# Kernel tuning notes

Hardware: AMD Instinct MI355X
Metric: run time of the kernel (lower is better)

Reference implementation:

```python
import jax, jax.numpy as jnp
import numpy as np

B_, L_, D_ = 8, 2048, 1024      # batch, seq_len, d_model
E, DS, K = 2, 16, 4             # expand, d_state, d_conv
DI = E * D_                     # d_inner = 2048
DTR = (D_ + 15) // 16           # dt_rank = 64


def setup_inputs() -> dict:
    key = jax.random.key(0)
    ks = jax.random.split(key, 8)
    g = lambda k, sh, sc=0.02: jax.random.normal(k, sh, jnp.float32) * sc
    return {
        "x": jax.random.normal(ks[0], (B_, L_, D_), jnp.float32),
        "ln_w": jnp.ones((D_,), jnp.float32),
        "ln_b": jnp.zeros((D_,), jnp.float32),
        "W_in": g(ks[1], (D_, 2 * DI)),
        "conv_w": g(ks[2], (DI, 1, K), 0.1),
        "conv_b": jnp.zeros((DI,), jnp.float32),
        "W_x": g(ks[3], (DI, DTR + 2 * DS)),
        "W_dt": g(ks[4], (DTR, DI), 0.1),
        "b_dt": jnp.full((DI,), -4.0, jnp.float32),  # softplus(-4) ~ 0.018 (small init dt)
        "A_log": jnp.log(jnp.broadcast_to(jnp.arange(1, DS + 1, dtype=jnp.float32), (DI, DS))),
        "Dp": jnp.ones((DI,), jnp.float32),
        "W_out": g(ks[5], (DI, D_)),
    }


def _mamba_block(x, ln_w, ln_b, W_in, conv_w, conv_b, W_x, W_dt, b_dt, A_log, Dp, W_out):
    # pre-norm
    mu = jnp.mean(x, axis=-1, keepdims=True)
    var = jnp.var(x, axis=-1, keepdims=True)
    xn = (x - mu) / jnp.sqrt(var + 1e-5) * ln_w + ln_b

    # input projection -> (u, z), each (B, L, DI)
    xz = jnp.einsum('bld,de->ble', xn, W_in)
    u, z = jnp.split(xz, 2, axis=-1)

    # causal depthwise conv1d along L
    uc = jax.lax.conv_general_dilated(
        u.transpose(0, 2, 1), conv_w, window_strides=(1,), padding=[(K - 1, 0)],
        feature_group_count=DI, dimension_numbers=('NCH', 'OIH', 'NCH'))
    u = jax.nn.silu(uc.transpose(0, 2, 1) + conv_b)

    # input-dependent SSM params
    xd = jnp.einsum('bld,de->ble', u, W_x)          # (B, L, DTR + 2*DS)
    dt = jax.nn.softplus(jnp.einsum('blr,rd->bld', xd[..., :DTR], W_dt) + b_dt)  # (B, L, DI)
    Bm = xd[..., DTR:DTR + DS]                       # (B, L, DS)
    Cm = xd[..., DTR + DS:]                          # (B, L, DS)
    A = -jnp.exp(A_log)                              # (DI, DS)

    # selective scan over time; carry h: (B, DI, DS)
    def step(h, inp):
        dt_t, u_t, B_t, C_t = inp                    # (B,DI),(B,DI),(B,DS),(B,DS)
        dA = jnp.exp(dt_t[..., None] * A)            # (B, DI, DS)
        h = h * dA + (dt_t * u_t)[..., None] * B_t[:, None, :]
        y = jnp.einsum('bds,bs->bd', h, C_t)
        return h, y

    h0 = jnp.zeros((x.shape[0], DI, DS), x.dtype)
    xs = (dt.transpose(1, 0, 2), u.transpose(1, 0, 2), Bm.transpose(1, 0, 2), Cm.transpose(1, 0, 2))
    _, ys = jax.lax.scan(step, h0, xs)               # ys: (L, B, DI)

    y = ys.transpose(1, 0, 2) + u * Dp
    y = y * jax.nn.silu(z)
    # output projection + residual (dropout is identity in eval)
    return jnp.einsum('bld,de->ble', y, W_out) + x


def reference(x, ln_w, ln_b, W_in, conv_w, conv_b, W_x, W_dt, b_dt, A_log, Dp, W_out):
    return _mamba_block(x, ln_w, ln_b, W_in, conv_w, conv_b, W_x, W_dt, b_dt, A_log, Dp, W_out)
```

## Files before the change

### kernel.cpp

```cpp
#include <hip/hip_runtime.h>

#define NB 8
#define NL 2048
#define ND 1024
#define NDI 2048
#define NDS 16
#define NDTR 64
#define NM (NB * NL)
#define CH 16
#define CL (NL / CH)

__device__ __forceinline__ float bf2f(unsigned int u) {
  union { unsigned int i; float f; } c; c.i = u << 16; return c.f;
}
__device__ __forceinline__ float lo16(unsigned int w) { return __uint_as_float(w << 16); }
__device__ __forceinline__ float hi16(unsigned int w) { return __uint_as_float(w & 0xffff0000u); }
__device__ __forceinline__ unsigned short f2bf(float f) {
  unsigned int x = __float_as_uint(f);
  x = x + 0x7fffu + ((x >> 16) & 1u);
  return (unsigned short)(x >> 16);
}
__device__ __forceinline__ void dec8(int4 raw, float* f) {
  f[0] = lo16((unsigned)raw.x); f[1] = hi16((unsigned)raw.x);
  f[2] = lo16((unsigned)raw.y); f[3] = hi16((unsigned)raw.y);
  f[4] = lo16((unsigned)raw.z); f[5] = hi16((unsigned)raw.z);
  f[6] = lo16((unsigned)raw.w); f[7] = hi16((unsigned)raw.w);
}
__device__ __forceinline__ float softplus_fast(float x) {
  return fmaxf(x, 0.f) + __logf(1.f + __expf(-fabsf(x)));
}

typedef __bf16 bf16x8 __attribute__((ext_vector_type(8)));
typedef float f32x4 __attribute__((ext_vector_type(4)));

__device__ __forceinline__ void gld_lds16(const unsigned short* g, unsigned short* l) {
  __builtin_amdgcn_global_load_lds(
      (const __attribute__((address_space(1))) unsigned int*)g,
      (__attribute__((address_space(3))) unsigned int*)l, 16, 0, 0);
}

__global__ __launch_bounds__(256) void k_ln(const float* __restrict__ x,
    const float* __restrict__ lw, const float* __restrict__ lb,
    unsigned short* __restrict__ xn)
{
  const int row = blockIdx.x;
  const int tid = threadIdx.x;
  const float* xr = x + (size_t)row * ND;
  float4 v = reinterpret_cast<const float4*>(xr)[tid];
  float s  = v.x + v.y + v.z + v.w;
  float s2 = v.x*v.x + v.y*v.y + v.z*v.z + v.w*v.w;
  #pragma unroll
  for (int m = 32; m >= 1; m >>= 1) {
    s  += __shfl_xor(s, m);
    s2 += __shfl_xor(s2, m);
  }
  __shared__ float red[8];
  const int wid = tid >> 6;
  if ((tid & 63) == 0) { red[wid] = s; red[4 + wid] = s2; }
  __syncthreads();
  s  = red[0] + red[1] + red[2] + red[3];
  s2 = red[4] + red[5] + red[6] + red[7];
  const float mu   = s * (1.0f / ND);
  const float var  = s2 * (1.0f / ND) - mu * mu;
  const float rstd = rsqrtf(var + 1e-5f);
  const float4 wv = reinterpret_cast<const float4*>(lw)[tid];
  const float4 bv = reinterpret_cast<const float4*>(lb)[tid];
  ushort4 o;
  o.x = f2bf((v.x - mu) * rstd * wv.x + bv.x);
  o.y = f2bf((v.y - mu) * rstd * wv.y + bv.y);
  o.z = f2bf((v.z - mu) * rstd * wv.z + bv.z);
  o.w = f2bf((v.w - mu) * rstd * wv.w + bv.w);
  reinterpret_cast<ushort4*>(xn + (size_t)row * ND)[tid] = o;
}

__global__ __launch_bounds__(256) void k_transpose(
    const float* __restrict__ W, unsigned short* __restrict__ WT,
    const int K, const int N)
{
  __shared__ float t[32][33];
  const int k0 = blockIdx.y * 32, n0 = blockIdx.x * 32;
  const int tx = threadIdx.x & 31, ty = threadIdx.x >> 5;
  #pragma unroll
  for (int r = 0; r < 4; ++r)
    t[ty + r * 8][tx] = W[(size_t)(k0 + ty + r * 8) * N + n0 + tx];
  __syncthreads();
  #pragma unroll
  for (int r = 0; r < 4; ++r)
    WT[(size_t)(n0 + ty + r * 8) * K + k0 + tx] = f2bf(t[tx][ty + r * 8]);
}

template<int MODE>
__global__ __launch_bounds__(512, 2) void k_mfma8(
    const unsigned short* __restrict__ A, const unsigned short* __restrict__ BT,
    const int K, const int N, void* __restrict__ O0, void* __restrict__ O1,
    const float* __restrict__ aux)
{
  __shared__ __align__(16) unsigned short sh[65536];
  const int tid = threadIdx.x, lane = tid & 63, wv = tid >> 6;
  const int wm = wv >> 2, wn = wv & 3;
  const int m16 = lane & 15, kb = lane >> 4;
  const int swzs = (((kb * 16) ^ (((m16 >> 1) & 3) << 4)) >> 1);
  const int arow = wm * 128 + m16;
  const int brow = wn * 64 + m16;

  int wg = blockIdx.x;
  const int cpx = gridDim.x >> 3;
  wg = (wg & 7) * cpx + (wg >> 3);
  const int gnx = N >> 8;
  const int m0 = (wg / gnx) << 8;
  const int n0 = (wg % gnx) << 8;

  f32x4 acc[8][4];
  #pragma unroll
  for (int i = 0; i < 8; ++i)
    #pragma unroll
    for (int j = 0; j < 4; ++j)
      #pragma unroll
      for (int r = 0; r < 4; ++r) acc[i][j][r] = 0.f;

  auto STAGE = [&](const unsigned short* X, int x0, int kg, unsigned short* base) {
    #pragma unroll
    for (int jj = 0; jj < 2; ++jj) {
      const int s = (wv * 2 + jj) * 64 + lane;
      const int row = s >> 2;
      const int c = (lane & 3) ^ ((row >> 1) & 3);
      gld_lds16(X + (size_t)(x0 + row) * K + kg + c * 8, base + (wv * 2 + jj) * 512);
    }
  };

#define PH(KH, FH, READB, STAGE_STMT, WAIT_STMT)                                \
  {                                                                             \
    bf16x8 aF[4];                                                               \
    const unsigned short* ab = sh + buf * 16384 + (KH) * 8192;                  \
    _Pragma("unroll")                                                           \
    for (int i = 0; i < 4; ++i)                                                 \
      aF[i] = *reinterpret_cast<const bf16x8*>(ab + (arow + (FH)*64 + i*16) * 32 + swzs); \
    if (READB) {                                                                \
      const unsigned short* bb = sh + 32768 + buf * 16384 + (KH) * 8192;        \
      _Pragma("unroll")                                                         \
      for (int j = 0; j < 4; ++j)                                               \
        bF[j] = *reinterpret_cast<const bf16x8*>(bb + (brow + j*16) * 32 + swzs); \
    }                                                                           \
    STAGE_STMT;                                                                 \
    WAIT_STMT;                                                                  \
    __builtin_amdgcn_s_barrier();                                               \
    asm volatile("s_waitcnt lgkmcnt(0)" ::: "memory");                          \
    __builtin_amdgcn_s_setprio(1);                                              \
    _Pragma("unroll")                                                           \
    for (int i = 0; i < 4; ++i)                                                 \
      _Pragma("unroll")                                                         \
      for (int j = 0; j < 4; ++j)                                               \
        acc[(FH)*4 + i][j] = __builtin_amdgcn_mfma_f32_16x16x32_bf16(aF[i], bF[j], acc[(FH)*4 + i][j], 0, 0, 0); \
    __builtin_amdgcn_s_setprio(0);                                              \
    __builtin_amdgcn_s_barrier();                                               \
  }

  STAGE(A,  m0, 0,  sh);
  STAGE(BT, n0, 0,  sh + 32768);
  STAGE(A,  m0, 32, sh + 8192);
  STAGE(BT, n0, 32, sh + 32768 + 8192);
  asm volatile("s_waitcnt vmcnt(0)" ::: "memory");
  __builtin_amdgcn_s_barrier();

  const int NT = K >> 6;
  for (int t = 0; t < NT; ++t) {
    const int buf = t & 1, nb = buf ^ 1;
    const int kn = (t << 6) + 64;
    const bool more = (t + 1 < NT);
    unsigned short* a0n = sh + nb * 16384;
    unsigned short* a1n = a0n + 8192;
    unsigned short* b0n = sh + 32768 + nb * 16384;
    unsigned short* b1n = b0n + 8192;
    bf16x8 bF[4];
    PH(0, 0, 1, if (more) STAGE(A, m0, kn, a0n), (void)0);
    PH(0, 1, 0, if (more) STAGE(BT, n0, kn, b0n),
       if (more) { asm volatile("s_waitcnt vmcnt(4)" ::: "memory"); }
       else      { asm volatile("s_waitcnt vmcnt(0)" ::: "memory"); });
    PH(1, 0, 1, if (more) STAGE(A, m0, kn + 32, a1n), (void)0);
    PH(1, 1, 0, if (more) STAGE(BT, n0, kn + 32, b1n),
       if (more) { asm volatile("s_waitcnt vmcnt(4)" ::: "memory"); });
  }
#undef PH

  {
    float* fsh = (float*)sh;
    constexpr int LDP = 260;
    const int erow = tid >> 4;
    const int ec0  = tid & 15;
    const int growb = m0 + (erow >> 4) * 128 + (erow & 15);
    #pragma unroll
    for (int i = 0; i < 8; ++i) {
      __builtin_amdgcn_s_barrier();
      #pragma unroll
      for (int j = 0; j < 4; ++j)
        #pragma unroll
        for (int r = 0; r < 4; ++r)
          fsh[(wm * 16 + kb * 4 + r) * LDP + wn * 64 + j * 16 + m16] = acc[i][j][r];
      __builtin_amdgcn_s_barrier();
      const int grow = growb + i * 16;
      #pragma unroll
      for (int q = 0; q < 4; ++q) {
        const int c = (ec0 + q * 16) * 4;
        float4 v = *reinterpret_cast<const float4*>(&fsh[erow * LDP + c]);
        const int colg = n0 + c;
        if constexpr (MODE == 0) {
          ushort4 o = {f2bf(v.x), f2bf(v.y), f2bf(v.z), f2bf(v.w)};
          unsigned short* dst = (colg < NDI)
              ? (unsigned short*)O0 + (size_t)grow * NDI + colg
              : (unsigned short*)O1 + (size_t)grow * NDI + colg - NDI;
          *reinterpret_cast<ushort4*>(dst) = o;
        } else {
          float4 rv = *reinterpret_cast<const float4*>(aux + (size_t)grow * N + colg);
          float4 o = {v.x + rv.x, v.y + rv.y, v.z + rv.z, v.w + rv.w};
          *reinterpret_cast<float4*>((float*)O0 + (size_t)grow * N + colg) = o;
        }
      }
    }
  }
  (void)O1; (void)aux;
}

__global__ __launch_bounds__(256) void k_mfma_dt(
    const unsigned short* __restrict__ A, const unsigned short* __restrict__ BT,
    const int K, void* __restrict__ O0, const float* __restrict__ aux, const int N)
{
  __shared__ __align__(16) unsigned short As[128 * 32];
  __shared__ __align__(16) unsigned short Bs[128 * 32];
  const int tid = threadIdx.x;
  const int lane = tid & 63;
  const int wv = tid >> 6;
  const int wm = wv >> 1, wn = wv & 1;
  const int m0 = blockIdx.y * 128, n0 = blockIdx.x * 128;
  const int m16 = lane & 15, kb = lane >> 4;
  const int wbase = wv * 64;

  f32x4 acc[4][4];
  #pragma unroll
  for (int i = 0; i < 4; ++i)
    #pragma unroll
    for (int j = 0; j < 4; ++j)
      #pragma unroll
      for (int r = 0; r < 4; ++r) acc[i][j][r] = 0.f;

  for (int k0 = 0; k0 < K; k0 += 32) {
    #pragma unroll
    for (int it = 0; it < 2; ++it) {
      const int c = it * 256 + tid;
      const int r = c >> 2, cb = c & 3;
      gld_lds16(A  + (size_t)(m0 + r) * K + k0 + cb * 8, As + (size_t)(it * 256 + wbase) * 8);
      gld_lds16(BT + (size_t)(n0 + r) * K + k0 + cb * 8, Bs + (size_t)(it * 256 + wbase) * 8);
    }
    __syncthreads();
    bf16x8 af[4], bfr[4];
    #pragma unroll
    for (int i = 0; i < 4; ++i)
      af[i] = *reinterpret_cast<const bf16x8*>(&As[(wm * 64 + i * 16 + m16) * 32 + kb * 8]);
    #pragma unroll
    for (int j = 0; j < 4; ++j)
      bfr[j] = *reinterpret_cast<const bf16x8*>(&Bs[(wn * 64 + j * 16 + m16) * 32 + kb * 8]);
    #pragma unroll
    for (int i = 0; i < 4; ++i)
      #pragma unroll
      for (int j = 0; j < 4; ++j)
        acc[i][j] = __builtin_amdgcn_mfma_f32_16x16x32_bf16(af[i], bfr[j], acc[i][j], 0, 0, 0);
    __syncthreads();
  }

  const int r0 = (lane >> 4) * 4;
  #pragma unroll
  for (int i = 0; i < 4; ++i) {
    const int rowb = m0 + wm * 64 + i * 16 + r0;
    #pragma unroll
    for (int j = 0; j < 4; ++j) {
      const int col = n0 + wn * 64 + j * 16 + m16;
      #pragma unroll
      for (int r = 0; r < 4; ++r) {
        const int row = rowb + r;
        ((unsigned short*)O0)[(size_t)row * N + col] =
            f2bf(softplus_fast(acc[i][j][r] + aux[col]));
      }
    }
  }
}

__global__ __launch_bounds__(256) void k_conv(
    const unsigned short* __restrict__ up, const float* __restrict__ cw,
    const float* __restrict__ cb, unsigned short* __restrict__ u)
{
  const int tid = threadIdx.x;
  const int c0 = tid * 8;
  const int lt = blockIdx.x & 127;
  const int b  = blockIdx.x >> 7;
  const int l0 = lt * 16;

  float4 wv[8];
  #pragma unroll
  for (int j = 0; j < 8; ++j)
    wv[j] = reinterpret_cast<const float4*>(cw + (size_t)c0 * 4)[j];
  float bias[8];
  {
    float4 b0 = reinterpret_cast<const float4*>(cb + c0)[0];
    float4 b1 = reinterpret_cast<const float4*>(cb + c0)[1];
    bias[0]=b0.x; bias[1]=b0.y; bias[2]=b0.z; bias[3]=b0.w;
    bias[4]=b1.x; bias[5]=b1.y; bias[6]=b1.z; bias[7]=b1.w;
  }

  const size_t base = ((size_t)b * NL + l0) * NDI + c0;
  float w0[8], w1[8], w2[8];
  if (l0 >= 3) {
    int4 r0 = *reinterpret_cast<const int4*>(up + base - 3 * NDI);
    int4 r1 = *reinterpret_cast<const int4*>(up + base - 2 * NDI);
    int4 r2 = *reinterpret_cast<const int4*>(up + base - 1 * NDI);
    dec8(r0, w0); dec8(r1, w1); dec8(r2, w2);
  } else {
    #pragma unroll
    for (int j = 0; j < 8; ++j) { w0[j] = 0.f; w1[j] = 0.f; w2[j] = 0.f; }
  }

  #pragma unroll
  for (int l = 0; l < 16; ++l) {
    int4 raw = *reinterpret_cast<const int4*>(up + base + (size_t)l * NDI);
    float cur[8];
    dec8(raw, cur);
    unsigned short o[8];
    #pragma unroll
    for (int j = 0; j < 8; ++j) {
      const float a = bias[j] + wv[j].x * w0[j] + wv[j].y * w1[j]
                              + wv[j].z * w2[j] + wv[j].w * cur[j];
      o[j] = f2bf(a / (1.f + __expf(-a)));
    }
    ushort4 o0 = {o[0], o[1], o[2], o[3]};
    ushort4 o1 = {o[4], o[5], o[6], o[7]};
    unsigned short* dst = u + base + (size_t)l * NDI;
    *reinterpret_cast<ushort4*>(dst)     = o0;
    *reinterpret_cast<ushort4*>(dst + 4) = o1;
    #pragma unroll
    for (int j = 0; j < 8; ++j) { w0[j] = w1[j]; w1[j] = w2[j]; w2[j] = cur[j]; }
  }
}

__global__ __launch_bounds__(256) void k_xd_mfma(
    const unsigned short* __restrict__ A, const unsigned short* __restrict__ BT,
    unsigned short* __restrict__ xdt, float* __restrict__ xb,
    float* __restrict__ xc)
{
  __shared__ __align__(16) unsigned short As[128 * 32];
  __shared__ __align__(16) unsigned short Bs[96 * 32];
  const int tid = threadIdx.x, lane = tid & 63, wv = tid >> 6;
  const int m0 = blockIdx.x * 128;
  const int m16 = lane & 15, kb = lane >> 4;
  f32x4 acc[2][6];
  #pragma unroll
  for (int i = 0; i < 2; ++i)
    #pragma unroll
    for (int j = 0; j < 6; ++j)
      #pragma unroll
      for (int r = 0; r < 4; ++r) acc[i][j][r] = 0.f;

  for (int k0 = 0; k0 < NDI; k0 += 32) {
    #pragma unroll
    for (int it = 0; it < 2; ++it) {
      const int slot = it * 256 + tid;
      const int r = slot >> 2, cb = slot & 3;
      gld_lds16(A + (size_t)(m0 + r) * NDI + k0 + cb * 8, As + (size_t)slot * 8);
      if (slot < 384)
        gld_lds16(BT + (size_t)r * NDI + k0 + cb * 8, Bs + (size_t)slot * 8);
    }
    __syncthreads();
    bf16x8 af[2], bfr[6];
    #pragma unroll
    for (int i = 0; i < 2; ++i)
      af[i] = *reinterpret_cast<const bf16x8*>(&As[(wv * 32 + i * 16 + m16) * 32 + kb * 8]);
    #pragma unroll
    for (int j = 0; j < 6; ++j)
      bfr[j] = *reinterpret_cast<const bf16x8*>(&Bs[(j * 16 + m16) * 32 + kb * 8]);
    #pragma unroll
    for (int i = 0; i < 2; ++i)
      #pragma unroll
      for (int j = 0; j < 6; ++j)
        acc[i][j] = __builtin_amdgcn_mfma_f32_16x16x32_bf16(af[i], bfr[j], acc[i][j], 0, 0, 0);
    __syncthreads();
  }
  const int r0 = (lane >> 4) * 4;
  #pragma unroll
  for (int i = 0; i < 2; ++i) {
    #pragma unroll
    for (int j = 0; j < 6; ++j) {
      const int col = j * 16 + m16;
      #pragma unroll
      for (int r = 0; r < 4; ++r) {
        const int row = m0 + wv * 32 + i * 16 + r0 + r;
        const float v = acc[i][j][r];
        if (j < 4)       xdt[(size_t)row * 64 + col] = f2bf(v);
        else if (j == 4) xb[(size_t)row * 16 + col - 64] = v;
        else             xc[(size_t)row * 16 + col - 80] = v;
      }
    }
  }
}

template<int PHASE>
__global__ __launch_bounds__(256) void k_scan3(
    const unsigned short* __restrict__ dt, unsigned short* __restrict__ u_io,
    const unsigned short* __restrict__ z,
    const float* __restrict__ xb, const float* __restrict__ xc,
    const float* __restrict__ A_log, const float* __restrict__ Dp,
    float* __restrict__ HF, float* __restrict__ Sdt)
{
  const int tid = threadIdx.x;
  const int blk = blockIdx.x;
  const int b = blk >> 7;
  const int c = (blk >> 3) & (CH - 1);
  if (PHASE == 0 && c == CH - 1) return;
  const int d = (blk & 7) * 256 + tid;

  __shared__ float Bsl[CL][16];
  __shared__ float Csl[(PHASE == 1) ? CL : 1][16];
  const size_t rbase = (size_t)b * NL + (size_t)c * CL;
  #pragma unroll
  for (int i = 0; i < 2; ++i) {
    const int idx = i * 256 + tid;
    const int r = idx >> 2, q = idx & 3;
    reinterpret_cast<float4*>(&Bsl[r][q * 4])[0] =
        reinterpret_cast<const float4*>(xb + (rbase + r) * 16)[q];
    if constexpr (PHASE == 1)
      reinterpret_cast<float4*>(&Csl[r][q * 4])[0] =
          reinterpret_cast<const float4*>(xc + (rbase + r) * 16)[q];
  }
  __syncthreads();

  float Ac[16];
  #pragma unroll
  for (int q = 0; q < 4; ++q) {
    float4 a = reinterpret_cast<const float4*>(A_log + (size_t)d * 16)[q];
    Ac[q*4+0] = -__expf(a.x); Ac[q*4+1] = -__expf(a.y);
    Ac[q*4+2] = -__expf(a.z); Ac[q*4+3] = -__expf(a.w);
  }
  bool fastok = true;
  #pragma unroll
  for (int s = 1; s < 16; ++s)
    fastok = fastok && (fabsf(Ac[s] - Ac[0] * (float)(s + 1)) <= 1e-5f * fabsf(Ac[s]));
  const bool fast = __all(fastok);

  const size_t hoff = ((size_t)(b * CH + c) * NDI + d) * 16;
  float h[16];
  if constexpr (PHASE == 0) {
    #pragma unroll
    for (int s = 0; s < 16; ++s) h[s] = 0.f;
  } else {
    #pragma unroll
    for (int q = 0; q < 4; ++q) {
      float4 hv = reinterpret_cast<const float4*>(HF + hoff)[q];
      h[q*4+0] = hv.x; h[q*4+1] = hv.y; h[q*4+2] = hv.z; h[q*4+3] = hv.w;
    }
  }
  const float Dd = Dp[d];
  const float Ac0 = Ac[0];
  float sdt = 0.f;
  size_t idx = rbase * NDI + d;

  if (fast) {
    for (int l = 0; l < CL; ++l, idx += NDI) {
      const float dtv = bf2f(dt[idx]);
      const float uv  = bf2f(u_io[idx]);
      const float dtu = dtv * uv;
      const float qq = __expf(dtv * Ac0);
      float e = qq;
      if constexpr (PHASE == 0) {
        sdt += dtv;
        #pragma unroll
        for (int s = 0; s < 16; ++s) {
          h[s] = h[s] * e + dtu * Bsl[l][s];
          e *= qq;
        }
      } else {
        float yp = 0.f;
        #pragma unroll
        for (int s = 0; s < 16; ++s) {
          h[s] = h[s] * e + dtu * Bsl[l][s];
          yp += h[s] * Csl[l][s];
          e *= qq;
        }
        const float zv = bf2f(z[idx]);
        const float sil = zv / (1.f + __expf(-zv));
        u_io[idx] = f2bf((yp + uv * Dd) * sil);
      }
    }
  } else {
    for (int l = 0; l < CL; ++l, idx += NDI) {
      const float dtv = bf2f(dt[idx]);
      const float uv  = bf2f(u_io[idx]);
      const float dtu = dtv * uv;
      if constexpr (PHASE == 0) {
        sdt += dtv;
        #pragma unroll
        for (int s = 0; s < 16; ++s) {
          const float e = __expf(dtv * Ac[s]);
          h[s] = h[s] * e + dtu * Bsl[l][s];
        }
      } else {
        float yp = 0.f;
        #pragma unroll
        for (int s = 0; s < 16; ++s) {
          const float e = __expf(dtv * Ac[s]);
          h[s] = h[s] * e + dtu * Bsl[l][s];
          yp += h[s] * Csl[l][s];
        }
        const float zv = bf2f(z[idx]);
        const float sil = zv / (1.f + __expf(-zv));
        u_io[idx] = f2bf((yp + uv * Dd) * sil);
      }
    }
  }

  if constexpr (PHASE == 0) {
    #pragma unroll
    for (int q = 0; q < 4; ++q) {
      float4 hv = {h[q*4+0], h[q*4+1], h[q*4+2], h[q*4+3]};
      reinterpret_cast<float4*>(HF + hoff)[q] = hv;
    }
    Sdt[(size_t)(b * CH + c) * NDI + d] = sdt;
  }
}

__global__ __launch_bounds__(256) void k_comb(
    float* __restrict__ HF, const float* __restrict__ Sdt,
    const float* __restrict__ A_log)
{
  const int t = blockIdx.x * 256 + threadIdx.x;
  const int b = t >> 15;
  const int q = t & 32767;
  const int d = q >> 4;
  const float Ac = -__expf(A_log[q]);
  float H = 0.f;
  #pragma unroll
  for (int c = 0; c < CH; ++c) {
    const size_t off = (((size_t)(b * CH + c) * NDI) << 4) + q;
    const float hf = HF[off];
    const float p  = __expf(Ac * Sdt[(size_t)(b * CH + c) * NDI + d]);
    HF[off] = H;
    H = p * H + hf;
  }
}

extern "C" void kernel_launch(void* const* d_in, const int* in_sizes, int n_in,
                              void* d_out, int out_size, void* d_ws, size_t ws_size,
                              hipStream_t stream) {
  (void)in_sizes; (void)n_in; (void)out_size; (void)ws_size;
  const float* x      = (const float*)d_in[0];
  const float* ln_w   = (const float*)d_in[1];
  const float* ln_b   = (const float*)d_in[2];
  const float* W_in   = (const float*)d_in[3];
  const float* conv_w = (const float*)d_in[4];
  const float* conv_b = (const float*)d_in[5];
  const float* W_x    = (const float*)d_in[6];
  const float* W_dt   = (const float*)d_in[7];
  const float* b_dt   = (const float*)d_in[8];
  const float* A_log  = (const float*)d_in[9];
  const float* Dp     = (const float*)d_in[10];
  const float* W_out  = (const float*)d_in[11];
  float* out = (float*)d_out;

  char* ws = (char*)d_ws;
  unsigned short* xn   = (unsigned short*)(ws);
  float*          HF   = (float*)(ws);
  unsigned short* upre = (unsigned short*)(ws + 33554432);
  unsigned short* zbuf = (unsigned short*)(ws + 100663296);
  unsigned short* ubuf = (unsigned short*)(ws + 167772160);
  unsigned short* xdt  = (unsigned short*)(ws + 234881024);
  float*          Sdt  = (float*)(ws + 234881024);
  float*          xb   = (float*)(ws + 236978176);
  float*          xc   = (float*)(ws + 238026752);
  unsigned short* WxT  = (unsigned short*)(ws + 239075328);
  unsigned short* WdtT = (unsigned short*)(ws + 239468544);
  unsigned short* WinT = (unsigned short*)(ws + 240123904);
  unsigned short* WoutT= (unsigned short*)(ws + 248512512);

  dim3 gt1(4096 / 32, 1024 / 32);
  k_transpose<<<gt1, 256, 0, stream>>>(W_in, WinT, 1024, 4096);
  dim3 gt2(1024 / 32, 2048 / 32);
  k_transpose<<<gt2, 256, 0, stream>>>(W_out, WoutT, 2048, 1024);
  dim3 gt3(96 / 32, 2048 / 32);
  k_transpose<<<gt3, 256, 0, stream>>>(W_x, WxT, 2048, 96);
  dim3 gt4(2048 / 32, 64 / 32);
  k_transpose<<<gt4, 256, 0, stream>>>(W_dt, WdtT, 64, 2048);

  k_ln<<<NM, 256, 0, stream>>>(x, ln_w, ln_b, xn);

  k_mfma8<0><<<(NM / 256) * (4096 / 256), 512, 0, stream>>>(
      xn, WinT, 1024, 4096, upre, zbuf, nullptr);

  k_conv<<<NB * (NL / 16), 256, 0, stream>>>(upre, conv_w, conv_b, ubuf);

  k_xd_mfma<<<NM / 128, 256, 0, stream>>>(ubuf, WxT, xdt, xb, xc);

  dim3 g3(2048 / 128, NM / 128);
  k_mfma_dt<<<g3, 256, 0, stream>>>(xdt, WdtT, 64, upre, b_dt, 2048);

  const int nscan = NB * CH * (NDI / 256);
  k_scan3<0><<<nscan, 256, 0, stream>>>(upre, ubuf, zbuf, xb, xc, A_log, Dp, HF, Sdt);
  k_comb<<<NB * NDI * NDS / 256, 256, 0, stream>>>(HF, Sdt, A_log);
  k_scan3<1><<<nscan, 256, 0, stream>>>(upre, ubuf, zbuf, xb, xc, A_log, Dp, HF, Sdt);

  k_mfma8<1><<<(NM / 256) * (1024 / 256), 512, 0, stream>>>(
      ubuf, WoutT, 2048, 1024, out, nullptr, x);
}
```

Measured before the change: 561.8 us.

## Software-pipeline LDS fragment reads ahead of MFMA in GEMM main loop

Restructures the GEMM k-loop so the LDS fragment reads for the next phase are issued before the current phase's MFMAs, using double-buffered register fragments (aA/aB, bA/bB). The previous version waited on lgkmcnt right before each MFMA group; now the reads overlap with matrix compute, and sched_barrier keeps the order fixed. This costs extra VGPRs for the duplicate fragments, which may lower occupancy, and the barrier placement has to stay correct for the double-buffered LDS.

```diff
diff --git a/kernel.cpp b/kernel.cpp
--- a/kernel.cpp
+++ b/kernel.cpp
@@ -127,33 +127,23 @@
       gld_lds16(X + (size_t)(x0 + row) * K + kg + c * 8, base + (wv * 2 + jj) * 512);
     }
   };
-
-#define PH(KH, FH, READB, STAGE_STMT, WAIT_STMT)                                \
-  {                                                                             \
-    bf16x8 aF[4];                                                               \
-    const unsigned short* ab = sh + buf * 16384 + (KH) * 8192;                  \
-    _Pragma("unroll")                                                           \
-    for (int i = 0; i < 4; ++i)                                                 \
-      aF[i] = *reinterpret_cast<const bf16x8*>(ab + (arow + (FH)*64 + i*16) * 32 + swzs); \
-    if (READB) {                                                                \
-      const unsigned short* bb = sh + 32768 + buf * 16384 + (KH) * 8192;        \
-      _Pragma("unroll")                                                         \
-      for (int j = 0; j < 4; ++j)                                               \
-        bF[j] = *reinterpret_cast<const bf16x8*>(bb + (brow + j*16) * 32 + swzs); \
-    }                                                                           \
-    STAGE_STMT;                                                                 \
-    WAIT_STMT;                                                                  \
-    __builtin_amdgcn_s_barrier();                                               \
-    asm volatile("s_waitcnt lgkmcnt(0)" ::: "memory");                          \
-    __builtin_amdgcn_s_setprio(1);                                              \
-    _Pragma("unroll")                                                           \
-    for (int i = 0; i < 4; ++i)                                                 \
-      _Pragma("unroll")                                                         \
-      for (int j = 0; j < 4; ++j)                                               \
-        acc[(FH)*4 + i][j] = __builtin_amdgcn_mfma_f32_16x16x32_bf16(aF[i], bF[j], acc[(FH)*4 + i][j], 0, 0, 0); \
-    __builtin_amdgcn_s_setprio(0);                                              \
-    __builtin_amdgcn_s_barrier();                                               \
-  }
+  auto RD_A = [&](bf16x8* dst, const unsigned short* base, int FH) {
+    #pragma unroll
+    for (int i = 0; i < 4; ++i)
+      dst[i] = *reinterpret_cast<const bf16x8*>(base + (arow + FH * 64 + i * 16) * 32 + swzs);
+  };
+  auto RD_B = [&](bf16x8* dst, const unsigned short* base) {
+    #pragma unroll
+    for (int j = 0; j < 4; ++j)
+      dst[j] = *reinterpret_cast<const bf16x8*>(base + (brow + j * 16) * 32 + swzs);
+  };
+  auto MM = [&](const bf16x8* aF, const bf16x8* bF, int off) {
+    #pragma unroll
+    for (int i = 0; i < 4; ++i)
+      #pragma unroll
+      for (int j = 0; j < 4; ++j)
+        acc[off + i][j] = __builtin_amdgcn_mfma_f32_16x16x32_bf16(aF[i], bF[j], acc[off + i][j], 0, 0, 0);
+  };
 
   STAGE(A,  m0, 0,  sh);
   STAGE(BT, n0, 0,  sh + 32768);
@@ -162,25 +152,50 @@
   asm volatile("s_waitcnt vmcnt(0)" ::: "memory");
   __builtin_amdgcn_s_barrier();
 
+  bf16x8 aA[4], aB[4], bA[4], bB[4];
+  RD_A(aA, sh, 0);
+  RD_B(bA, sh + 32768);
+
   const int NT = K >> 6;
   for (int t = 0; t < NT; ++t) {
     const int buf = t & 1, nb = buf ^ 1;
     const int kn = (t << 6) + 64;
     const bool more = (t + 1 < NT);
-    unsigned short* a0n = sh + nb * 16384;
-    unsigned short* a1n = a0n + 8192;
-    unsigned short* b0n = sh + 32768 + nb * 16384;
-    unsigned short* b1n = b0n + 8192;
-    bf16x8 bF[4];
-    PH(0, 0, 1, if (more) STAGE(A, m0, kn, a0n), (void)0);
-    PH(0, 1, 0, if (more) STAGE(BT, n0, kn, b0n),
-       if (more) { asm volatile("s_waitcnt vmcnt(4)" ::: "memory"); }
-       else      { asm volatile("s_waitcnt vmcnt(0)" ::: "memory"); });
-    PH(1, 0, 1, if (more) STAGE(A, m0, kn + 32, a1n), (void)0);
-    PH(1, 1, 0, if (more) STAGE(BT, n0, kn + 32, b1n),
-       if (more) { asm volatile("s_waitcnt vmcnt(4)" ::: "memory"); });
-  }
-#undef PH
+    const unsigned short* cA = sh + buf * 16384;
+    const unsigned short* cB = sh + 32768 + buf * 16384;
+    unsigned short* nA = sh + nb * 16384;
+    unsigned short* nB = sh + 32768 + nb * 16384;
+
+    if (more) STAGE(A, m0, kn, nA);
+    RD_A(aB, cA, 1);
+    __builtin_amdgcn_sched_barrier(0);
+    __builtin_amdgcn_s_setprio(1); MM(aA, bA, 0); __builtin_amdgcn_s_setprio(0);
+    __builtin_amdgcn_s_barrier();
+
+    if (more) STAGE(BT, n0, kn, nB);
+    if (more) { asm volatile("s_waitcnt vmcnt(4)" ::: "memory"); }
+    else      { asm volatile("s_waitcnt vmcnt(0)" ::: "memory"); }
+    __builtin_amdgcn_s_barrier();
+    RD_A(aA, cA + 8192, 0);
+    RD_B(bB, cB + 8192);
+    __builtin_amdgcn_sched_barrier(0);
+    __builtin_amdgcn_s_setprio(1); MM(aB, bA, 4); __builtin_amdgcn_s_setprio(0);
+    __builtin_amdgcn_s_barrier();
+
+    if (more) STAGE(A, m0, kn + 32, nA + 8192);
+    RD_A(aB, cA + 8192, 1);
+    __builtin_amdgcn_sched_barrier(0);
+    __builtin_amdgcn_s_setprio(1); MM(aA, bB, 0); __builtin_amdgcn_s_setprio(0);
+    __builtin_amdgcn_s_barrier();
+
+    if (more) STAGE(BT, n0, kn + 32, nB + 8192);
+    if (more) asm volatile("s_waitcnt vmcnt(4)" ::: "memory");
+    __builtin_amdgcn_s_barrier();
+    if (more) { RD_A(aA, nA, 0); RD_B(bA, nB); }
+    __builtin_amdgcn_sched_barrier(0);
+    __builtin_amdgcn_s_setprio(1); MM(aB, bB, 4); __builtin_amdgcn_s_setprio(0);
+    __builtin_amdgcn_s_barrier();
+  }
 
   {
     float* fsh = (float*)sh;
```

After: 546.8 us. 1.03x faster.
